# Optimization experiments

Hardware: AMD Instinct MI355X
Metric: run time of the kernel (lower is better)

The kernel has to match this reference:

```python
import jax, jax.numpy as jnp
import numpy as np

H = 1024          # hiddenSize
V = 50257         # outputSize (vocab)
L = 512           # maxLength (encoder length)


def setup_inputs() -> dict:
    key = jax.random.key(0)
    ks = jax.random.split(key, 16)
    s = 0.02
    return {
        "input": jax.random.randint(ks[0], (1,), 0, V),
        "hidden": jax.random.normal(ks[1], (1, 1, H), jnp.float32),
        "encoder_outputs": jax.random.normal(ks[2], (L, H), jnp.float32),
        "emb": jax.random.normal(ks[3], (V, H), jnp.float32) * s,
        "W_attn": jax.random.normal(ks[4], (L, 2 * H), jnp.float32) * s,
        "b_attn": jnp.zeros((L,), jnp.float32),
        "W_comb": jax.random.normal(ks[5], (H, 2 * H), jnp.float32) * s,
        "b_comb": jnp.zeros((H,), jnp.float32),
        "W_ih": jax.random.normal(ks[6], (3 * H, H), jnp.float32) * s,
        "W_hh": jax.random.normal(ks[7], (3 * H, H), jnp.float32) * s,
        "b_ih": jnp.zeros((3 * H,), jnp.float32),
        "b_hh": jnp.zeros((3 * H,), jnp.float32),
        "W_out": jax.random.normal(ks[8], (V, H), jnp.float32) * s,
        "b_out": jnp.zeros((V,), jnp.float32),
    }


def reference(input, hidden, encoder_outputs, emb, W_attn, b_attn,
              W_comb, b_comb, W_ih, W_hh, b_ih, b_hh, W_out, b_out):
    # embedding lookup: [1, H] (dropout p=0 -> identity)
    embedded = emb[input]
    h = hidden[0]                                   # [1, H]
    # attention over encoder positions
    attn_logits = jnp.concatenate([embedded, h], axis=1) @ W_attn.T + b_attn
    attn_weights = jax.nn.softmax(attn_logits, axis=1)      # [1, L]
    attn_applied = attn_weights @ encoder_outputs           # [1, H]
    # combine and relu
    x = jnp.concatenate([embedded, attn_applied], axis=1) @ W_comb.T + b_comb
    x = jax.nn.relu(x)                                      # [1, H]
    # single GRU step (PyTorch gate layout: r, z, n)
    gi = x @ W_ih.T + b_ih                                  # [1, 3H]
    gh = h @ W_hh.T + b_hh                                  # [1, 3H]
    i_r, i_z, i_n = jnp.split(gi, 3, axis=1)
    h_r, h_z, h_n = jnp.split(gh, 3, axis=1)
    r = jax.nn.sigmoid(i_r + h_r)
    z = jax.nn.sigmoid(i_z + h_z)
    n = jnp.tanh(i_n + r * h_n)
    h_new = (1.0 - z) * n + z * h                           # [1, H]
    # output distribution
    output = jax.nn.log_softmax(h_new @ W_out.T + b_out, axis=1)  # [1, V]
    return output, h_new[None], attn_weights
```

## Files before the change

kernel.cpp:

```cpp
#include <hip/hip_runtime.h>
#include <cmath>

#define H 1024
#define V 50257
#define L 512
#define NB5 1571

__device__ __forceinline__ float wred_sum(float v) {
#pragma unroll
    for (int o = 32; o > 0; o >>= 1) v += __shfl_xor(v, o, 64);
    return v;
}
__device__ __forceinline__ float dot4(float4 a, float4 b) {
    return a.x * b.x + a.y * b.y + a.z * b.z + a.w * b.w;
}
__device__ __forceinline__ void ms_merge(float& m, float& s, float m2, float s2) {
    float M = fmaxf(m, m2);
    if (M == -INFINITY) { m = M; s = 0.f; return; }
    s = s * expf(m - M) + s2 * expf(m2 - M);
    m = M;
}

__global__ void k_phase1(const int* __restrict__ tok,
                         const float* __restrict__ hid,
                         const float* __restrict__ emb,
                         const float* __restrict__ Wa,
                         const float* __restrict__ ba,
                         const float* __restrict__ enc,
                         const float* __restrict__ Whh,
                         const float* __restrict__ bhh,
                         float* __restrict__ num4,
                         float* __restrict__ Sacc,
                         float* __restrict__ elg,
                         float* __restrict__ gh) {
    const int t = threadIdx.x;
    const int lane = t & 63, wv = t >> 6;
    const float4* h4 = (const float4*)hid;
    if (blockIdx.x < 128) {
        const int l = blockIdx.x * 4 + wv;
        const float4* e4 = (const float4*)(emb + (size_t)tok[0] * H);
        const float4* wr = (const float4*)(Wa + (size_t)l * 2048);
        float acc = 0.f;
#pragma unroll
        for (int k = 0; k < 8; ++k) {
            int f = 64 * k + lane;
            float4 s = (f < 256) ? e4[f] : h4[f - 256];
            acc += dot4(wr[f], s);
        }
        acc = wred_sum(acc);
        const float e = expf(acc + ba[l]);
        __shared__ float se[4];
        if (lane == 0) { se[wv] = e; elg[l] = e; }
        __syncthreads();
        if (t == 0) atomicAdd(Sacc, se[0] + se[1] + se[2] + se[3]);
        float4 a = make_float4(0.f, 0.f, 0.f, 0.f);
#pragma unroll
        for (int r = 0; r < 4; ++r) {
            const float w = se[r];
            const float4 v = ((const float4*)(enc + (size_t)(blockIdx.x * 4 + r) * H))[t];
            a.x += w * v.x; a.y += w * v.y; a.z += w * v.z; a.w += w * v.w;
        }
        float* dst = num4 + (size_t)(blockIdx.x & 3) * 1024 + 4 * t;
        atomicAdd(dst + 0, a.x);
        atomicAdd(dst + 1, a.y);
        atomicAdd(dst + 2, a.z);
        atomicAdd(dst + 3, a.w);
    } else {
        const int j = (blockIdx.x - 128) * 4 + wv;
        const float4* wh = (const float4*)(Whh + (size_t)j * H);
        float acc = 0.f;
#pragma unroll
        for (int k = 0; k < 4; ++k) {
            int f = 64 * k + lane;
            acc += dot4(wh[f], h4[f]);
        }
        acc = wred_sum(acc);
        if (lane == 0) gh[j] = acc + bhh[j];
    }
}

__global__ void k_comb(const int* __restrict__ tok,
                       const float* __restrict__ emb,
                       const float* __restrict__ num4,
                       const float* __restrict__ Sacc,
                       const float* __restrict__ elg,
                       const float* __restrict__ Wc,
                       const float* __restrict__ bcb,
                       float* __restrict__ xv,
                       float* __restrict__ wout) {
    const int t = threadIdx.x;
    const int lane = t & 63, wv = t >> 6;
    const int j = blockIdx.x * 4 + wv;
    const float invS = 1.f / Sacc[0];
    const float4* e4 = (const float4*)(emb + (size_t)tok[0] * H);
    const float4* n4 = (const float4*)num4;
    const float4* wr = (const float4*)(Wc + (size_t)j * 2048);
    float acc = 0.f;
#pragma unroll
    for (int k = 0; k < 4; ++k) {
        int f = 64 * k + lane;
        acc += dot4(wr[f], e4[f]);
        float4 s0 = n4[f], s1 = n4[256 + f], s2 = n4[512 + f], s3 = n4[768 + f];
        float4 aa = make_float4((s0.x + s1.x + s2.x + s3.x) * invS,
                                (s0.y + s1.y + s2.y + s3.y) * invS,
                                (s0.z + s1.z + s2.z + s3.z) * invS,
                                (s0.w + s1.w + s2.w + s3.w) * invS);
        acc += dot4(wr[256 + f], aa);
    }
    acc = wred_sum(acc);
    if (lane == 0) xv[j] = fmaxf(acc + bcb[j], 0.f);
    if (blockIdx.x == 0) {
        wout[t] = elg[t] * invS;
        wout[t + 256] = elg[t + 256] * invS;
    }
}

__global__ void k_gates_gru(const float* __restrict__ xv,
                            const float* __restrict__ hid,
                            const float* __restrict__ Wih,
                            const float* __restrict__ bih,
                            const float* __restrict__ gh,
                            float* __restrict__ hn_out,
                            float* __restrict__ hn_ws) {
    const int lane = threadIdx.x & 63, wv = threadIdx.x >> 6;
    const int j = blockIdx.x * 4 + wv;
    const float4* x4 = (const float4*)xv;
    float4 xreg[4];
#pragma unroll
    for (int k = 0; k < 4; ++k) xreg[k] = x4[64 * k + lane];
    float g[3];
#pragma unroll
    for (int p = 0; p < 3; ++p) {
        const float4* wr = (const float4*)(Wih + (size_t)(j + p * H) * H);
        float acc = 0.f;
#pragma unroll
        for (int k = 0; k < 4; ++k) acc += dot4(wr[64 * k + lane], xreg[k]);
        g[p] = wred_sum(acc) + bih[j + p * H];
    }
    if (lane == 0) {
        float r = 1.f / (1.f + expf(-(g[0] + gh[j])));
        float z = 1.f / (1.f + expf(-(g[1] + gh[j + H])));
        float n = tanhf(g[2] + r * gh[j + 2 * H]);
        float hv = (1.f - z) * n + z * hid[j];
        hn_out[j] = hv;
        hn_ws[j] = hv;
    }
}

__global__ void k_out_gemv(const float* __restrict__ hn,
                           const float* __restrict__ Wo,
                           const float* __restrict__ bo,
                           float* __restrict__ logits,
                           float* __restrict__ pm,
                           float* __restrict__ ps) {
    const int lane = threadIdx.x & 63, wv = threadIdx.x >> 6;
    const int b = blockIdx.x;
    const float4* h4 = (const float4*)hn;
    float4 hreg[4];
#pragma unroll
    for (int k = 0; k < 4; ++k) hreg[k] = h4[64 * k + lane];
    float lv[8];
    int nvalid = 0;
#pragma unroll
    for (int i = 0; i < 8; ++i) {
        const int v = b * 32 + wv * 8 + i;
        if (v < V) {
            const float4* wr = (const float4*)(Wo + (size_t)v * H);
            float acc = 0.f;
#pragma unroll
            for (int k = 0; k < 4; ++k) acc += dot4(wr[64 * k + lane], hreg[k]);
            acc = wred_sum(acc) + bo[v];
            if (lane == 0) logits[v] = acc;
            lv[nvalid++] = acc;
        }
    }
    float m = -INFINITY, s = 0.f;
    for (int i = 0; i < nvalid; ++i) m = fmaxf(m, lv[i]);
    for (int i = 0; i < nvalid; ++i) s += expf(lv[i] - m);
    __shared__ float smm[4], sms[4];
    if (lane == 0) { smm[wv] = m; sms[wv] = s; }
    __syncthreads();
    if (threadIdx.x == 0) {
        float M = smm[0], S = sms[0];
#pragma unroll
        for (int i = 1; i < 4; ++i) ms_merge(M, S, smm[i], sms[i]);
        pm[b] = M; ps[b] = S;
    }
}

__global__ void k_finalize(float* __restrict__ out,
                           const float* __restrict__ pm,
                           const float* __restrict__ ps) {
    const int t = threadIdx.x;
    const int lane = t & 63, wv = t >> 6;
    float m = -INFINITY, s = 0.f;
    for (int i = t; i < NB5; i += 256) ms_merge(m, s, pm[i], ps[i]);
#pragma unroll
    for (int o = 32; o > 0; o >>= 1) {
        float m2 = __shfl_xor(m, o, 64);
        float s2 = __shfl_xor(s, o, 64);
        ms_merge(m, s, m2, s2);
    }
    __shared__ float smm[4], sms[4];
    __shared__ float Cs;
    if (lane == 0) { smm[wv] = m; sms[wv] = s; }
    __syncthreads();
    if (t == 0) {
        float M = smm[0], S = sms[0];
#pragma unroll
        for (int i = 1; i < 4; ++i) ms_merge(M, S, smm[i], sms[i]);
        Cs = M + logf(S);
    }
    __syncthreads();
    const float C = Cs;
    const int v = blockIdx.x * 256 + t;
    if (v < V) out[v] -= C;
}

extern "C" void kernel_launch(void* const* d_in, const int* in_sizes, int n_in,
                              void* d_out, int out_size, void* d_ws, size_t ws_size,
                              hipStream_t stream) {
    const int*   tok = (const int*)d_in[0];
    const float* hid = (const float*)d_in[1];
    const float* enc = (const float*)d_in[2];
    const float* emb = (const float*)d_in[3];
    const float* Wa  = (const float*)d_in[4];
    const float* ba  = (const float*)d_in[5];
    const float* Wc  = (const float*)d_in[6];
    const float* bc  = (const float*)d_in[7];
    const float* Wih = (const float*)d_in[8];
    const float* Whh = (const float*)d_in[9];
    const float* bih = (const float*)d_in[10];
    const float* bhh = (const float*)d_in[11];
    const float* Wo  = (const float*)d_in[12];
    const float* bo  = (const float*)d_in[13];

    float* out = (float*)d_out;
    float* ws  = (float*)d_ws;
    float* num4 = ws;
    float* Sacc = ws + 4096;
    float* elg  = ws + 4112;
    float* gh   = ws + 4624;
    float* xv   = ws + 7696;
    float* hn   = ws + 8720;
    float* pm   = ws + 9744;
    float* psum = ws + 11316;

    float* out_logits = out;
    float* out_hnew   = out + V;
    float* out_attnw  = out + V + H;

    hipMemsetAsync(ws, 0, 4097 * sizeof(float), stream);
    k_phase1<<<896, 256, 0, stream>>>(tok, hid, emb, Wa, ba, enc, Whh, bhh,
                                      num4, Sacc, elg, gh);
    k_comb<<<256, 256, 0, stream>>>(tok, emb, num4, Sacc, elg, Wc, bc, xv, out_attnw);
    k_gates_gru<<<256, 256, 0, stream>>>(xv, hid, Wih, bih, gh, out_hnew, hn);
    k_out_gemv<<<NB5, 256, 0, stream>>>(hn, Wo, bo, out_logits, pm, psum);
    k_finalize<<<197, 256, 0, stream>>>(out_logits, pm, psum);
}
```

Before: 66.11 us.

## Fuse all stages into one persistent kernel with software grid barriers

Replaces the five separate launches with a single persistent kernel whose grid is sized from occupancy and capped at 1024 blocks. The stages (attention logits plus Whh GEMV, attention apply, combine, GRU gates, output GEMV with online softmax, finalize) are separated by software grid barriers built on spread-out atomic counters. The work split also changes: combine and gate rows become per-block instead of per-wave. This removes launch gaps and inter-kernel drains, but every barrier costs a global spin, and correctness depends on all blocks being co-resident, which a normal launch does not guarantee.

```diff
diff --git a/kernel.cpp b/kernel.cpp
--- a/kernel.cpp
+++ b/kernel.cpp
@@ -4,7 +4,17 @@
 #define H 1024
 #define V 50257
 #define L 512
-#define NB5 1571
+#define MAXNB 1024
+
+struct Args {
+    const int* tok; const float* hid; const float* enc; const float* emb;
+    const float* Wa; const float* ba; const float* Wc; const float* bcb;
+    const float* Wih; const float* bih; const float* Whh; const float* bhh;
+    const float* Wo; const float* bo;
+    float* elg; float* gh; float* aa; float* xv; float* hn;
+    float* pm; float* ps; unsigned* bar;
+    float* out_logits; float* out_hnew; float* out_attnw;
+};
 
 __device__ __forceinline__ float wred_sum(float v) {
 #pragma unroll
@@ -21,240 +31,223 @@
     m = M;
 }
 
-__global__ void k_phase1(const int* __restrict__ tok,
-                         const float* __restrict__ hid,
-                         const float* __restrict__ emb,
-                         const float* __restrict__ Wa,
-                         const float* __restrict__ ba,
-                         const float* __restrict__ enc,
-                         const float* __restrict__ Whh,
-                         const float* __restrict__ bhh,
-                         float* __restrict__ num4,
-                         float* __restrict__ Sacc,
-                         float* __restrict__ elg,
-                         float* __restrict__ gh) {
-    const int t = threadIdx.x;
-    const int lane = t & 63, wv = t >> 6;
-    const float4* h4 = (const float4*)hid;
-    if (blockIdx.x < 128) {
-        const int l = blockIdx.x * 4 + wv;
-        const float4* e4 = (const float4*)(emb + (size_t)tok[0] * H);
-        const float4* wr = (const float4*)(Wa + (size_t)l * 2048);
-        float acc = 0.f;
-#pragma unroll
-        for (int k = 0; k < 8; ++k) {
-            int f = 64 * k + lane;
-            float4 s = (f < 256) ? e4[f] : h4[f - 256];
-            acc += dot4(wr[f], s);
-        }
-        acc = wred_sum(acc);
-        const float e = expf(acc + ba[l]);
-        __shared__ float se[4];
-        if (lane == 0) { se[wv] = e; elg[l] = e; }
-        __syncthreads();
-        if (t == 0) atomicAdd(Sacc, se[0] + se[1] + se[2] + se[3]);
-        float4 a = make_float4(0.f, 0.f, 0.f, 0.f);
-#pragma unroll
-        for (int r = 0; r < 4; ++r) {
-            const float w = se[r];
-            const float4 v = ((const float4*)(enc + (size_t)(blockIdx.x * 4 + r) * H))[t];
-            a.x += w * v.x; a.y += w * v.y; a.z += w * v.z; a.w += w * v.w;
-        }
-        float* dst = num4 + (size_t)(blockIdx.x & 3) * 1024 + 4 * t;
-        atomicAdd(dst + 0, a.x);
-        atomicAdd(dst + 1, a.y);
-        atomicAdd(dst + 2, a.z);
-        atomicAdd(dst + 3, a.w);
-    } else {
-        const int j = (blockIdx.x - 128) * 4 + wv;
-        const float4* wh = (const float4*)(Whh + (size_t)j * H);
-        float acc = 0.f;
-#pragma unroll
-        for (int k = 0; k < 4; ++k) {
-            int f = 64 * k + lane;
-            acc += dot4(wh[f], h4[f]);
-        }
-        acc = wred_sum(acc);
-        if (lane == 0) gh[j] = acc + bhh[j];
-    }
-}
-
-__global__ void k_comb(const int* __restrict__ tok,
-                       const float* __restrict__ emb,
-                       const float* __restrict__ num4,
-                       const float* __restrict__ Sacc,
-                       const float* __restrict__ elg,
-                       const float* __restrict__ Wc,
-                       const float* __restrict__ bcb,
-                       float* __restrict__ xv,
-                       float* __restrict__ wout) {
-    const int t = threadIdx.x;
-    const int lane = t & 63, wv = t >> 6;
-    const int j = blockIdx.x * 4 + wv;
-    const float invS = 1.f / Sacc[0];
-    const float4* e4 = (const float4*)(emb + (size_t)tok[0] * H);
-    const float4* n4 = (const float4*)num4;
-    const float4* wr = (const float4*)(Wc + (size_t)j * 2048);
-    float acc = 0.f;
-#pragma unroll
-    for (int k = 0; k < 4; ++k) {
-        int f = 64 * k + lane;
-        acc += dot4(wr[f], e4[f]);
-        float4 s0 = n4[f], s1 = n4[256 + f], s2 = n4[512 + f], s3 = n4[768 + f];
-        float4 aa = make_float4((s0.x + s1.x + s2.x + s3.x) * invS,
-                                (s0.y + s1.y + s2.y + s3.y) * invS,
-                                (s0.z + s1.z + s2.z + s3.z) * invS,
-                                (s0.w + s1.w + s2.w + s3.w) * invS);
-        acc += dot4(wr[256 + f], aa);
-    }
-    acc = wred_sum(acc);
-    if (lane == 0) xv[j] = fmaxf(acc + bcb[j], 0.f);
-    if (blockIdx.x == 0) {
-        wout[t] = elg[t] * invS;
-        wout[t + 256] = elg[t + 256] * invS;
-    }
-}
-
-__global__ void k_gates_gru(const float* __restrict__ xv,
-                            const float* __restrict__ hid,
-                            const float* __restrict__ Wih,
-                            const float* __restrict__ bih,
-                            const float* __restrict__ gh,
-                            float* __restrict__ hn_out,
-                            float* __restrict__ hn_ws) {
-    const int lane = threadIdx.x & 63, wv = threadIdx.x >> 6;
-    const int j = blockIdx.x * 4 + wv;
-    const float4* x4 = (const float4*)xv;
-    float4 xreg[4];
-#pragma unroll
-    for (int k = 0; k < 4; ++k) xreg[k] = x4[64 * k + lane];
-    float g[3];
-#pragma unroll
-    for (int p = 0; p < 3; ++p) {
-        const float4* wr = (const float4*)(Wih + (size_t)(j + p * H) * H);
-        float acc = 0.f;
-#pragma unroll
-        for (int k = 0; k < 4; ++k) acc += dot4(wr[64 * k + lane], xreg[k]);
-        g[p] = wred_sum(acc) + bih[j + p * H];
-    }
-    if (lane == 0) {
-        float r = 1.f / (1.f + expf(-(g[0] + gh[j])));
-        float z = 1.f / (1.f + expf(-(g[1] + gh[j + H])));
-        float n = tanhf(g[2] + r * gh[j + 2 * H]);
-        float hv = (1.f - z) * n + z * hid[j];
-        hn_out[j] = hv;
-        hn_ws[j] = hv;
-    }
-}
-
-__global__ void k_out_gemv(const float* __restrict__ hn,
-                           const float* __restrict__ Wo,
-                           const float* __restrict__ bo,
-                           float* __restrict__ logits,
-                           float* __restrict__ pm,
-                           float* __restrict__ ps) {
-    const int lane = threadIdx.x & 63, wv = threadIdx.x >> 6;
-    const int b = blockIdx.x;
-    const float4* h4 = (const float4*)hn;
-    float4 hreg[4];
-#pragma unroll
-    for (int k = 0; k < 4; ++k) hreg[k] = h4[64 * k + lane];
-    float lv[8];
-    int nvalid = 0;
-#pragma unroll
-    for (int i = 0; i < 8; ++i) {
-        const int v = b * 32 + wv * 8 + i;
-        if (v < V) {
-            const float4* wr = (const float4*)(Wo + (size_t)v * H);
-            float acc = 0.f;
-#pragma unroll
-            for (int k = 0; k < 4; ++k) acc += dot4(wr[64 * k + lane], hreg[k]);
-            acc = wred_sum(acc) + bo[v];
-            if (lane == 0) logits[v] = acc;
-            lv[nvalid++] = acc;
-        }
-    }
-    float m = -INFINITY, s = 0.f;
-    for (int i = 0; i < nvalid; ++i) m = fmaxf(m, lv[i]);
-    for (int i = 0; i < nvalid; ++i) s += expf(lv[i] - m);
-    __shared__ float smm[4], sms[4];
-    if (lane == 0) { smm[wv] = m; sms[wv] = s; }
+__device__ __forceinline__ void gbar(unsigned* bar, int ph, unsigned nblk) {
     __syncthreads();
     if (threadIdx.x == 0) {
-        float M = smm[0], S = sms[0];
-#pragma unroll
-        for (int i = 1; i < 4; ++i) ms_merge(M, S, smm[i], sms[i]);
-        pm[b] = M; ps[b] = S;
-    }
-}
-
-__global__ void k_finalize(float* __restrict__ out,
-                           const float* __restrict__ pm,
-                           const float* __restrict__ ps) {
-    const int t = threadIdx.x;
-    const int lane = t & 63, wv = t >> 6;
-    float m = -INFINITY, s = 0.f;
-    for (int i = t; i < NB5; i += 256) ms_merge(m, s, pm[i], ps[i]);
-#pragma unroll
-    for (int o = 32; o > 0; o >>= 1) {
-        float m2 = __shfl_xor(m, o, 64);
-        float s2 = __shfl_xor(s, o, 64);
-        ms_merge(m, s, m2, s2);
-    }
-    __shared__ float smm[4], sms[4];
-    __shared__ float Cs;
-    if (lane == 0) { smm[wv] = m; sms[wv] = s; }
+        __threadfence();
+        unsigned* c = bar + ph * 512;
+        __hip_atomic_fetch_add(&c[(blockIdx.x & 15) * 32], 1u,
+                               __ATOMIC_RELAXED, __HIP_MEMORY_SCOPE_AGENT);
+        unsigned sum;
+        do {
+            sum = 0;
+#pragma unroll
+            for (int i = 0; i < 16; ++i)
+                sum += __hip_atomic_load(&c[i * 32], __ATOMIC_RELAXED,
+                                         __HIP_MEMORY_SCOPE_AGENT);
+            if (sum < nblk) __builtin_amdgcn_s_sleep(2);
+        } while (sum < nblk);
+        __threadfence();
+    }
     __syncthreads();
-    if (t == 0) {
-        float M = smm[0], S = sms[0];
-#pragma unroll
-        for (int i = 1; i < 4; ++i) ms_merge(M, S, smm[i], sms[i]);
-        Cs = M + logf(S);
-    }
-    __syncthreads();
-    const float C = Cs;
-    const int v = blockIdx.x * 256 + t;
-    if (v < V) out[v] -= C;
+}
+
+__global__ __launch_bounds__(256, 4) void mega(Args args) {
+    const int t = threadIdx.x, lane = t & 63, wv = t >> 6, b = blockIdx.x;
+    const unsigned nblk = gridDim.x;
+    const int nw = nblk * 4;
+    const int gw = b * 4 + wv;
+    const float4* h4 = (const float4*)args.hid;
+    const float4* e4 = (const float4*)(args.emb + (size_t)args.tok[0] * H);
+    __shared__ float s_a[4], s_b[4], s_g[3][4];
+    __shared__ float s_c;
+
+    for (int job = gw; job < 3588; job += nw) {
+        if (job < 512) {
+            const float4* wr = (const float4*)(args.Wa + (size_t)job * 2048);
+            float acc = 0.f;
+#pragma unroll
+            for (int k = 0; k < 8; ++k) {
+                int f = 64 * k + lane;
+                float4 s = (f < 256) ? e4[f] : h4[f - 256];
+                acc += dot4(wr[f], s);
+            }
+            acc = wred_sum(acc);
+            if (lane == 0) args.elg[job] = expf(acc + args.ba[job]);
+        } else if (job < 3584) {
+            const int j = job - 512;
+            const float4* wh = (const float4*)(args.Whh + (size_t)j * H);
+            float acc = 0.f;
+#pragma unroll
+            for (int k = 0; k < 4; ++k) {
+                int f = 64 * k + lane;
+                acc += dot4(wh[f], h4[f]);
+            }
+            acc = wred_sum(acc);
+            if (lane == 0) args.gh[j] = acc + args.bhh[j];
+        } else {
+            ((float4*)args.aa)[(job - 3584) * 64 + lane] =
+                make_float4(0.f, 0.f, 0.f, 0.f);
+        }
+    }
+    gbar(args.bar, 0, nblk);
+
+    if (b <= 32) {
+        float e0 = args.elg[t], e1 = args.elg[t + 256];
+        float s = wred_sum(e0 + e1);
+        if (lane == 0) s_a[wv] = s;
+        __syncthreads();
+        const float invS = 1.f / (s_a[0] + s_a[1] + s_a[2] + s_a[3]);
+        if (b < 32) {
+            float4 a = make_float4(0.f, 0.f, 0.f, 0.f);
+#pragma unroll 4
+            for (int l = b * 16; l < b * 16 + 16; ++l) {
+                const float w = args.elg[l] * invS;
+                const float4 v = ((const float4*)(args.enc + (size_t)l * H))[t];
+                a.x += w * v.x; a.y += w * v.y; a.z += w * v.z; a.w += w * v.w;
+            }
+            float* dst = args.aa + 4 * t;
+            atomicAdd(dst + 0, a.x);
+            atomicAdd(dst + 1, a.y);
+            atomicAdd(dst + 2, a.z);
+            atomicAdd(dst + 3, a.w);
+        } else {
+            args.out_attnw[t] = e0 * invS;
+            args.out_attnw[t + 256] = e1 * invS;
+        }
+    }
+    gbar(args.bar, 1, nblk);
+
+    {
+        const float4* a4 = (const float4*)args.aa;
+        for (int j = b; j < H; j += nblk) {
+            const float4* wr = (const float4*)(args.Wc + (size_t)j * 2048);
+            float acc = dot4(wr[t], e4[t]) + dot4(wr[t + 256], a4[t]);
+            acc = wred_sum(acc);
+            if (lane == 0) s_a[wv] = acc;
+            __syncthreads();
+            if (t == 0)
+                args.xv[j] = fmaxf(s_a[0] + s_a[1] + s_a[2] + s_a[3] +
+                                   args.bcb[j], 0.f);
+            __syncthreads();
+        }
+    }
+    gbar(args.bar, 2, nblk);
+
+    {
+        const float4 xr = ((const float4*)args.xv)[t];
+        for (int j = b; j < H; j += nblk) {
+            float g0 = dot4(((const float4*)(args.Wih + (size_t)j * H))[t], xr);
+            float g1 = dot4(((const float4*)(args.Wih + (size_t)(j + H) * H))[t], xr);
+            float g2 = dot4(((const float4*)(args.Wih + (size_t)(j + 2 * H) * H))[t], xr);
+            g0 = wred_sum(g0); g1 = wred_sum(g1); g2 = wred_sum(g2);
+            if (lane == 0) { s_g[0][wv] = g0; s_g[1][wv] = g1; s_g[2][wv] = g2; }
+            __syncthreads();
+            if (t == 0) {
+                float G0 = s_g[0][0] + s_g[0][1] + s_g[0][2] + s_g[0][3] + args.bih[j];
+                float G1 = s_g[1][0] + s_g[1][1] + s_g[1][2] + s_g[1][3] + args.bih[j + H];
+                float G2 = s_g[2][0] + s_g[2][1] + s_g[2][2] + s_g[2][3] + args.bih[j + 2 * H];
+                float r = 1.f / (1.f + expf(-(G0 + args.gh[j])));
+                float z = 1.f / (1.f + expf(-(G1 + args.gh[j + H])));
+                float n = tanhf(G2 + r * args.gh[j + 2 * H]);
+                float hv = (1.f - z) * n + z * args.hid[j];
+                args.hn[j] = hv;
+                args.out_hnew[j] = hv;
+            }
+            __syncthreads();
+        }
+    }
+    gbar(args.bar, 3, nblk);
+
+    {
+        float4 hreg[4];
+#pragma unroll
+        for (int k = 0; k < 4; ++k) hreg[k] = ((const float4*)args.hn)[64 * k + lane];
+        float m = -INFINITY, s = 0.f;
+        for (int v = gw; v < V; v += nw) {
+            const float4* wr = (const float4*)(args.Wo + (size_t)v * H);
+            float acc = 0.f;
+#pragma unroll
+            for (int k = 0; k < 4; ++k) acc += dot4(wr[64 * k + lane], hreg[k]);
+            acc = wred_sum(acc) + args.bo[v];
+            if (lane == 0) args.out_logits[v] = acc;
+            float M = fmaxf(m, acc);
+            s = s * expf(m - M) + expf(acc - M);
+            m = M;
+        }
+        if (lane == 0) { s_a[wv] = m; s_b[wv] = s; }
+        __syncthreads();
+        if (t == 0) {
+            float M = s_a[0], S = s_b[0];
+#pragma unroll
+            for (int i = 1; i < 4; ++i) ms_merge(M, S, s_a[i], s_b[i]);
+            args.pm[b] = M; args.ps[b] = S;
+        }
+    }
+    gbar(args.bar, 4, nblk);
+
+    {
+        float m2 = -INFINITY, s2 = 0.f;
+        for (int i = t; i < (int)nblk; i += 256) ms_merge(m2, s2, args.pm[i], args.ps[i]);
+#pragma unroll
+        for (int o = 32; o > 0; o >>= 1) {
+            float mo = __shfl_xor(m2, o, 64), so = __shfl_xor(s2, o, 64);
+            ms_merge(m2, s2, mo, so);
+        }
+        if (lane == 0) { s_a[wv] = m2; s_b[wv] = s2; }
+        __syncthreads();
+        if (t == 0) {
+            float M = s_a[0], S = s_b[0];
+#pragma unroll
+            for (int i = 1; i < 4; ++i) ms_merge(M, S, s_a[i], s_b[i]);
+            s_c = M + logf(S);
+        }
+        __syncthreads();
+        const float C = s_c;
+        for (int v = b * 256 + t; v < V; v += nblk * 256)
+            args.out_logits[v] -= C;
+    }
 }
 
 extern "C" void kernel_launch(void* const* d_in, const int* in_sizes, int n_in,
                               void* d_out, int out_size, void* d_ws, size_t ws_size,
                               hipStream_t stream) {
-    const int*   tok = (const int*)d_in[0];
-    const float* hid = (const float*)d_in[1];
-    const float* enc = (const float*)d_in[2];
-    const float* emb = (const float*)d_in[3];
-    const float* Wa  = (const float*)d_in[4];
-    const float* ba  = (const float*)d_in[5];
-    const float* Wc  = (const float*)d_in[6];
-    const float* bc  = (const float*)d_in[7];
-    const float* Wih = (const float*)d_in[8];
-    const float* Whh = (const float*)d_in[9];
-    const float* bih = (const float*)d_in[10];
-    const float* bhh = (const float*)d_in[11];
-    const float* Wo  = (const float*)d_in[12];
-    const float* bo  = (const float*)d_in[13];
+    Args a;
+    a.tok = (const int*)d_in[0];
+    a.hid = (const float*)d_in[1];
+    a.enc = (const float*)d_in[2];
+    a.emb = (const float*)d_in[3];
+    a.Wa  = (const float*)d_in[4];
+    a.ba  = (const float*)d_in[5];
+    a.Wc  = (const float*)d_in[6];
+    a.bcb = (const float*)d_in[7];
+    a.Wih = (const float*)d_in[8];
+    a.Whh = (const float*)d_in[9];
+    a.bih = (const float*)d_in[10];
+    a.bhh = (const float*)d_in[11];
+    a.Wo  = (const float*)d_in[12];
+    a.bo  = (const float*)d_in[13];
 
     float* out = (float*)d_out;
     float* ws  = (float*)d_ws;
-    float* num4 = ws;
-    float* Sacc = ws + 4096;
-    float* elg  = ws + 4112;
-    float* gh   = ws + 4624;
-    float* xv   = ws + 7696;
-    float* hn   = ws + 8720;
-    float* pm   = ws + 9744;
-    float* psum = ws + 11316;
-
-    float* out_logits = out;
-    float* out_hnew   = out + V;
-    float* out_attnw  = out + V + H;
-
-    hipMemsetAsync(ws, 0, 4097 * sizeof(float), stream);
-    k_phase1<<<896, 256, 0, stream>>>(tok, hid, emb, Wa, ba, enc, Whh, bhh,
-                                      num4, Sacc, elg, gh);
-    k_comb<<<256, 256, 0, stream>>>(tok, emb, num4, Sacc, elg, Wc, bc, xv, out_attnw);
-    k_gates_gru<<<256, 256, 0, stream>>>(xv, hid, Wih, bih, gh, out_hnew, hn);
-    k_out_gemv<<<NB5, 256, 0, stream>>>(hn, Wo, bo, out_logits, pm, psum);
-    k_finalize<<<197, 256, 0, stream>>>(out_logits, pm, psum);
-}
+    a.elg = ws;
+    a.gh  = ws + 512;
+    a.aa  = ws + 3584;
+    a.xv  = ws + 4608;
+    a.hn  = ws + 5632;
+    a.pm  = ws + 6656;
+    a.ps  = ws + 7680;
+    a.bar = (unsigned*)(ws + 8704);
+    a.out_logits = out;
+    a.out_hnew   = out + V;
+    a.out_attnw  = out + V + H;
+
+    int occ = 0;
+    hipOccupancyMaxActiveBlocksPerMultiprocessor(&occ, mega, 256, 0);
+    if (occ < 1) occ = 1;
+    unsigned nblk = (unsigned)occ * 256u;
+    if (nblk > MAXNB) nblk = MAXNB;
+
+    hipMemsetAsync(a.bar, 0, 5 * 512 * sizeof(unsigned), stream);
+    mega<<<nblk, 256, 0, stream>>>(a);
+}
```

New measurement: 176.5 us. +166.9%, slower.

## Replace atomic attention accumulation with per-block partials reduced in combine kernel

Applied to the files above, without the earlier changes.

Attention-weighted encoder sums are now written as per-block float4 partials into a workspace buffer instead of atomically added into four shared copies. The softmax denominator is recomputed in every combine block from the stored exponentials, so the memset launch and the atomic counter are removed. The W_hh blocks now handle three rows per wave, which shrinks the phase-1 grid. The trade-off is that each of the 256 combine blocks re-reads 512 KB of partials, adding redundant L2 traffic to a kernel on the critical path.

```diff
diff --git a/kernel.cpp b/kernel.cpp
--- a/kernel.cpp
+++ b/kernel.cpp
@@ -5,6 +5,7 @@
 #define V 50257
 #define L 512
 #define NB5 1571
+#define NPART 128
 
 __device__ __forceinline__ float wred_sum(float v) {
 #pragma unroll
@@ -29,15 +30,13 @@
                          const float* __restrict__ enc,
                          const float* __restrict__ Whh,
                          const float* __restrict__ bhh,
-                         float* __restrict__ num4,
-                         float* __restrict__ Sacc,
                          float* __restrict__ elg,
+                         float* __restrict__ pbuf,
                          float* __restrict__ gh) {
-    const int t = threadIdx.x;
-    const int lane = t & 63, wv = t >> 6;
+    const int t = threadIdx.x, lane = t & 63, wv = t >> 6, b = blockIdx.x;
     const float4* h4 = (const float4*)hid;
-    if (blockIdx.x < 128) {
-        const int l = blockIdx.x * 4 + wv;
+    if (b < NPART) {
+        const int l = b * 4 + wv;
         const float4* e4 = (const float4*)(emb + (size_t)tok[0] * H);
         const float4* wr = (const float4*)(Wa + (size_t)l * 2048);
         float acc = 0.f;
@@ -52,67 +51,70 @@
         __shared__ float se[4];
         if (lane == 0) { se[wv] = e; elg[l] = e; }
         __syncthreads();
-        if (t == 0) atomicAdd(Sacc, se[0] + se[1] + se[2] + se[3]);
         float4 a = make_float4(0.f, 0.f, 0.f, 0.f);
 #pragma unroll
         for (int r = 0; r < 4; ++r) {
             const float w = se[r];
-            const float4 v = ((const float4*)(enc + (size_t)(blockIdx.x * 4 + r) * H))[t];
+            const float4 v = ((const float4*)(enc + (size_t)(b * 4 + r) * H))[t];
             a.x += w * v.x; a.y += w * v.y; a.z += w * v.z; a.w += w * v.w;
         }
-        float* dst = num4 + (size_t)(blockIdx.x & 3) * 1024 + 4 * t;
-        atomicAdd(dst + 0, a.x);
-        atomicAdd(dst + 1, a.y);
-        atomicAdd(dst + 2, a.z);
-        atomicAdd(dst + 3, a.w);
+        ((float4*)pbuf)[b * 256 + t] = a;
     } else {
-        const int j = (blockIdx.x - 128) * 4 + wv;
-        const float4* wh = (const float4*)(Whh + (size_t)j * H);
-        float acc = 0.f;
-#pragma unroll
-        for (int k = 0; k < 4; ++k) {
-            int f = 64 * k + lane;
-            acc += dot4(wh[f], h4[f]);
-        }
-        acc = wred_sum(acc);
-        if (lane == 0) gh[j] = acc + bhh[j];
+        const int base = (b - NPART) * 12 + wv * 3;
+#pragma unroll
+        for (int r = 0; r < 3; ++r) {
+            const int j = base + r;
+            const float4* wh = (const float4*)(Whh + (size_t)j * H);
+            float acc = 0.f;
+#pragma unroll
+            for (int k = 0; k < 4; ++k) {
+                int f = 64 * k + lane;
+                acc += dot4(wh[f], h4[f]);
+            }
+            acc = wred_sum(acc);
+            if (lane == 0) gh[j] = acc + bhh[j];
+        }
     }
 }
 
 __global__ void k_comb(const int* __restrict__ tok,
                        const float* __restrict__ emb,
-                       const float* __restrict__ num4,
-                       const float* __restrict__ Sacc,
                        const float* __restrict__ elg,
+                       const float* __restrict__ pbuf,
                        const float* __restrict__ Wc,
                        const float* __restrict__ bcb,
                        float* __restrict__ xv,
                        float* __restrict__ wout) {
-    const int t = threadIdx.x;
-    const int lane = t & 63, wv = t >> 6;
-    const int j = blockIdx.x * 4 + wv;
-    const float invS = 1.f / Sacc[0];
+    const int t = threadIdx.x, lane = t & 63, wv = t >> 6, b = blockIdx.x;
+    __shared__ float red[4];
+    __shared__ float4 aaL[256];
+    const float e0 = elg[t], e1 = elg[t + 256];
+    float s = wred_sum(e0 + e1);
+    if (lane == 0) red[wv] = s;
+    __syncthreads();
+    const float invS = 1.f / (red[0] + red[1] + red[2] + red[3]);
+    float4 a = make_float4(0.f, 0.f, 0.f, 0.f);
+#pragma unroll 8
+    for (int i = 0; i < NPART; ++i) {
+        const float4 p = ((const float4*)pbuf)[i * 256 + t];
+        a.x += p.x; a.y += p.y; a.z += p.z; a.w += p.w;
+    }
+    a.x *= invS; a.y *= invS; a.z *= invS; a.w *= invS;
+    aaL[t] = a;
+    __syncthreads();
+    if (b == 0) { wout[t] = e0 * invS; wout[t + 256] = e1 * invS; }
+    const int j = b * 4 + wv;
     const float4* e4 = (const float4*)(emb + (size_t)tok[0] * H);
-    const float4* n4 = (const float4*)num4;
     const float4* wr = (const float4*)(Wc + (size_t)j * 2048);
     float acc = 0.f;
 #pragma unroll
     for (int k = 0; k < 4; ++k) {
         int f = 64 * k + lane;
         acc += dot4(wr[f], e4[f]);
-        float4 s0 = n4[f], s1 = n4[256 + f], s2 = n4[512 + f], s3 = n4[768 + f];
-        float4 aa = make_float4((s0.x + s1.x + s2.x + s3.x) * invS,
-                                (s0.y + s1.y + s2.y + s3.y) * invS,
-                                (s0.z + s1.z + s2.z + s3.z) * invS,
-                                (s0.w + s1.w + s2.w + s3.w) * invS);
-        acc += dot4(wr[256 + f], aa);
+        acc += dot4(wr[256 + f], aaL[f]);
     }
     acc = wred_sum(acc);
     if (lane == 0) xv[j] = fmaxf(acc + bcb[j], 0.f);
-    if (blockIdx.x == 0) {
-        wout[t] = elg[t] * invS;
-        wout[t + 256] = elg[t + 256] * invS;
-    }
 }
 
 __global__ void k_gates_gru(const float* __restrict__ xv,
@@ -191,8 +193,7 @@
 __global__ void k_finalize(float* __restrict__ out,
                            const float* __restrict__ pm,
                            const float* __restrict__ ps) {
-    const int t = threadIdx.x;
-    const int lane = t & 63, wv = t >> 6;
+    const int t = threadIdx.x, lane = t & 63, wv = t >> 6;
     float m = -INFINITY, s = 0.f;
     for (int i = t; i < NB5; i += 256) ms_merge(m, s, pm[i], ps[i]);
 #pragma unroll
@@ -237,23 +238,21 @@
 
     float* out = (float*)d_out;
     float* ws  = (float*)d_ws;
-    float* num4 = ws;
-    float* Sacc = ws + 4096;
-    float* elg  = ws + 4112;
-    float* gh   = ws + 4624;
-    float* xv   = ws + 7696;
-    float* hn   = ws + 8720;
-    float* pm   = ws + 9744;
-    float* psum = ws + 11316;
+    float* elg  = ws;
+    float* gh   = ws + 512;
+    float* xv   = ws + 3584;
+    float* hn   = ws + 4608;
+    float* pm   = ws + 5632;
+    float* psum = ws + 7203;
+    float* pbuf = ws + 8832;
 
     float* out_logits = out;
     float* out_hnew   = out + V;
     float* out_attnw  = out + V + H;
 
-    hipMemsetAsync(ws, 0, 4097 * sizeof(float), stream);
-    k_phase1<<<896, 256, 0, stream>>>(tok, hid, emb, Wa, ba, enc, Whh, bhh,
-                                      num4, Sacc, elg, gh);
-    k_comb<<<256, 256, 0, stream>>>(tok, emb, num4, Sacc, elg, Wc, bc, xv, out_attnw);
+    k_phase1<<<384, 256, 0, stream>>>(tok, hid, emb, Wa, ba, enc, Whh, bhh,
+                                      elg, pbuf, gh);
+    k_comb<<<256, 256, 0, stream>>>(tok, emb, elg, pbuf, Wc, bc, xv, out_attnw);
     k_gates_gru<<<256, 256, 0, stream>>>(xv, hid, Wih, bih, gh, out_hnew, hn);
     k_out_gemv<<<NB5, 256, 0, stream>>>(hn, Wo, bo, out_logits, pm, psum);
     k_finalize<<<197, 256, 0, stream>>>(out_logits, pm, psum);
```

Result: faster. 64.61 us (-2.3%).
